# Performance work log

Hardware: AMD Instinct MI355X
Metric: run time of the kernel (lower is better)

Reference implementation:

```python
import jax, jax.numpy as jnp
import numpy as np

B, N, D = 2, 4096, 512
H, P = 8, 9            # num_heads, n_points
HD = D // H            # head_dim
OFFSET_SCALE = 4.0


def setup_inputs() -> dict:
    key = jax.random.key(0)
    ks = jax.random.split(key, 8)
    g = lambda k, shape, s: jax.random.normal(k, shape, jnp.float32) * s
    return {
        "x": jax.random.normal(ks[0], (B, N, D), jnp.float32),
        "Wq": g(ks[1], (D, D), 0.02),
        "bq": jnp.zeros((D,), jnp.float32),
        # offset predictor (original inits to zero; randomized small for a nontrivial test)
        "Woff": g(ks[2], (H * P * 2, D), 0.05),
        "boff": g(ks[3], (H * P * 2,), 0.05),
        # 1x1 conv producing k/v maps == a D -> 2D linear on tokens
        "Wkv": g(ks[4], (2 * D, D), 0.02),
        "bkv": jnp.zeros((2 * D,), jnp.float32),
        "Wo": g(ks[5], (D, D), 0.02),
        "bo": jnp.zeros((D,), jnp.float32),
        "h": 16,
        "w": 256,
    }


def _bilinear_zeros(feat, sx, sy, h, w):
    """grid_sample(mode=bilinear, padding=zeros, align_corners=True).
    feat: (B, H, N, hd) with N = h*w row-major; sx, sy: (B, H, S) pixel coords.
    Returns (B, H, S, hd). (align_corners=True normalize/denormalize round-trip
    in the original is the identity, so we sample at pixel coords directly.)
    """
    x0 = jnp.floor(sx)
    y0 = jnp.floor(sy)
    wx1 = sx - x0
    wy1 = sy - y0

    def corner(xi, yi, wgt):
        valid = ((xi >= 0) & (xi < w) & (yi >= 0) & (yi < h)).astype(feat.dtype)
        idx = (jnp.clip(yi, 0, h - 1) * w + jnp.clip(xi, 0, w - 1)).astype(jnp.int32)
        val = jnp.take_along_axis(feat, idx[..., None], axis=2)  # (B,H,S,hd)
        return val * (wgt * valid)[..., None]

    return (corner(x0, y0, (1 - wx1) * (1 - wy1))
            + corner(x0 + 1, y0, wx1 * (1 - wy1))
            + corner(x0, y0 + 1, (1 - wx1) * wy1)
            + corner(x0 + 1, y0 + 1, wx1 * wy1))


def reference(x, Wq, bq, Woff, boff, Wkv, bkv, Wo, bo, h, w):
    b, n, d = x.shape
    # queries, split heads -> (B,H,N,hd)
    q = (x @ Wq.T + bq).reshape(b, n, H, HD).transpose(0, 2, 1, 3)
    # per-query, per-head offsets in pixels: (B,N,H,P,2) (dx,dy)
    off = jnp.tanh(x @ Woff.T + boff).reshape(b, n, H, P, 2) * OFFSET_SCALE
    # 1x1 conv -> k/v token maps, split heads -> (B,H,N,hd)
    kv = x @ Wkv.T + bkv
    k = kv[..., :d].reshape(b, n, H, HD).transpose(0, 2, 1, 3)
    v = kv[..., d:].reshape(b, n, H, HD).transpose(0, 2, 1, 3)
    # base pixel grid (x,y) per token
    tok = jnp.arange(n)
    base = jnp.stack([(tok % w).astype(x.dtype), (tok // w).astype(x.dtype)], -1)  # (N,2)
    samp = base[None, :, None, None, :] + off          # (B,N,H,P,2)
    samp = samp.transpose(0, 2, 1, 3, 4).reshape(b, H, n * P, 2)
    sk = _bilinear_zeros(k, samp[..., 0], samp[..., 1], h, w).reshape(b, H, n, P, HD)
    sv = _bilinear_zeros(v, samp[..., 0], samp[..., 1], h, w).reshape(b, H, n, P, HD)
    logits = jnp.einsum('bhnd,bhnpd->bhnp', q, sk) * (HD ** -0.5)
    attn = jax.nn.softmax(logits, axis=-1)
    out = jnp.einsum('bhnp,bhnpd->bhnd', attn, sv)
    out = out.transpose(0, 2, 1, 3).reshape(b, n, d)   # merge heads
    return out @ Wo.T + bo
```

## Files before the change

### kernel.cpp

```cpp
#include <hip/hip_runtime.h>
#include <hip/hip_bf16.h>

static constexpr int B_  = 2;
static constexpr int N_  = 4096;
static constexpr int D_  = 512;
static constexpr int H_  = 8;
static constexpr int P_  = 9;
static constexpr int GH_ = 16;
static constexpr int GW_ = 256;
static constexpr int M_  = B_ * N_;

typedef __attribute__((ext_vector_type(8))) short bf16x8;
typedef __attribute__((ext_vector_type(4))) float f32x4;

__device__ __forceinline__ unsigned short f2b(float f) {
    __hip_bfloat16 h = __float2bfloat16(f);
    return *reinterpret_cast<unsigned short*>(&h);
}
__device__ __forceinline__ float b2f(unsigned short u) {
    return __uint_as_float(((unsigned int)u) << 16);
}
__device__ __forceinline__ float b2f_lo(unsigned int u) { return __uint_as_float(u << 16); }
__device__ __forceinline__ float b2f_hi(unsigned int u) { return __uint_as_float(u & 0xffff0000u); }

__global__ __launch_bounds__(256) void cast_multi(
    const float* __restrict__ x,   const float* __restrict__ wq,
    const float* __restrict__ wkv, const float* __restrict__ wo,
    const float* __restrict__ woff,
    unsigned short* __restrict__ x_hi, unsigned short* __restrict__ x_lo,
    unsigned short* __restrict__ wall, unsigned short* __restrict__ wob) {
    int g = blockIdx.x * 256 + threadIdx.x;

    if (g < 1048576) {
        float4 v = reinterpret_cast<const float4*>(x)[g];
        ushort4 hi, lo;
        hi.x = f2b(v.x); hi.y = f2b(v.y); hi.z = f2b(v.z); hi.w = f2b(v.w);
        lo.x = f2b(v.x - b2f(hi.x)); lo.y = f2b(v.y - b2f(hi.y));
        lo.z = f2b(v.z - b2f(hi.z)); lo.w = f2b(v.w - b2f(hi.w));
        reinterpret_cast<ushort4*>(x_hi)[g] = hi;
        reinterpret_cast<ushort4*>(x_lo)[g] = lo;
        return;
    }
    g -= 1048576;
    if (g < 65536) {
        float4 v = reinterpret_cast<const float4*>(wq)[g];
        ushort4 o; o.x = f2b(v.x); o.y = f2b(v.y); o.z = f2b(v.z); o.w = f2b(v.w);
        reinterpret_cast<ushort4*>(wall)[g] = o;
        return;
    }
    g -= 65536;
    if (g < 131072) {
        float4 v = reinterpret_cast<const float4*>(wkv)[g];
        ushort4 o; o.x = f2b(v.x); o.y = f2b(v.y); o.z = f2b(v.z); o.w = f2b(v.w);
        reinterpret_cast<ushort4*>(wall)[65536 + g] = o;
        return;
    }
    g -= 131072;
    if (g < 65536) {
        float4 v = reinterpret_cast<const float4*>(wo)[g];
        ushort4 o; o.x = f2b(v.x); o.y = f2b(v.y); o.z = f2b(v.z); o.w = f2b(v.w);
        reinterpret_cast<ushort4*>(wob)[g] = o;
        return;
    }
    g -= 65536;
    if (g < 18432) {
        float4 v = reinterpret_cast<const float4*>(woff)[g];
        ushort4 hi, lo;
        hi.x = f2b(v.x); hi.y = f2b(v.y); hi.z = f2b(v.z); hi.w = f2b(v.w);
        lo.x = f2b(v.x - b2f(hi.x)); lo.y = f2b(v.y - b2f(hi.y));
        lo.z = f2b(v.z - b2f(hi.z)); lo.w = f2b(v.w - b2f(hi.w));
        reinterpret_cast<ushort4*>(wall)[196608 + g] = hi;
        reinterpret_cast<ushort4*>(wall)[229376 + g] = lo;
        reinterpret_cast<ushort4*>(wall)[262144 + g] = hi;
        return;
    }
    g -= 18432;
    const int which = g / 14336;
    const int idx   = g - which * 14336;
    ushort4 z = {0, 0, 0, 0};
    reinterpret_cast<ushort4*>(wall)[215040 + which * 32768 + idx] = z;
}

__device__ __forceinline__ void gemm_seg(const unsigned short* __restrict__ A,
                                         const unsigned short* __restrict__ W,
                                         int m0, int n0, int Kloop, int lda, int ldw,
                                         short* As, short* Bs,
                                         f32x4 (&acc)[4][2], int wave, int lane) {
    const int gi = wave * 64 + lane;
    const int r0 = gi >> 2, c0 = (gi & 3) * 8;

    const unsigned short* pa0 = A + (size_t)(m0 + r0) * lda + c0;
    const unsigned short* pa1 = A + (size_t)(m0 + 64 + r0) * lda + c0;
    const unsigned short* pw  = W + (size_t)(n0 + r0) * ldw + c0;

    short* ldsA0 = As + wave * 512;
    short* ldsA1 = As + 2048 + wave * 512;
    short* ldsB  = Bs + wave * 512;

    const int wm = wave & 1, wn = wave >> 1;
    const int fr = lane & 15;
    const int fk = (lane >> 4) * 8;

    for (int k0 = 0; k0 < Kloop; k0 += 32) {
        __builtin_amdgcn_global_load_lds(
            (const __attribute__((address_space(1))) void*)(pa0 + k0),
            (__attribute__((address_space(3))) void*)ldsA0, 16, 0, 0);
        __builtin_amdgcn_global_load_lds(
            (const __attribute__((address_space(1))) void*)(pa1 + k0),
            (__attribute__((address_space(3))) void*)ldsA1, 16, 0, 0);
        __builtin_amdgcn_global_load_lds(
            (const __attribute__((address_space(1))) void*)(pw + k0),
            (__attribute__((address_space(3))) void*)ldsB, 16, 0, 0);
        __syncthreads();

        bf16x8 af[4], bf[2];
#pragma unroll
        for (int i = 0; i < 4; ++i)
            af[i] = *reinterpret_cast<const bf16x8*>(
                &As[(wm * 64 + i * 16 + fr) * 32 + fk]);
#pragma unroll
        for (int j = 0; j < 2; ++j)
            bf[j] = *reinterpret_cast<const bf16x8*>(
                &Bs[(wn * 32 + j * 16 + fr) * 32 + fk]);
#pragma unroll
        for (int i = 0; i < 4; ++i)
#pragma unroll
            for (int j = 0; j < 2; ++j)
                acc[i][j] = __builtin_amdgcn_mfma_f32_16x16x32_bf16(
                    af[i], bf[j], acc[i][j], 0, 0, 0);
        __syncthreads();
    }
}

__global__ __launch_bounds__(256, 3) void gemm_fused(
    const unsigned short* __restrict__ x_hi,
    const unsigned short* __restrict__ x_lo,
    const unsigned short* __restrict__ wall,
    const float* __restrict__ bq,
    const float* __restrict__ bkv,
    const float* __restrict__ boff,
    unsigned short* __restrict__ q_bf,
    unsigned short* __restrict__ k_bf,
    unsigned short* __restrict__ v_bf,
    float* __restrict__ off1,
    float* __restrict__ off2,
    float* __restrict__ off3) {
    __shared__ short As[4096];
    __shared__ short Bs[2048];
    const int t = threadIdx.x;
    const int wave = t >> 6, lane = t & 63;
    const int m0 = blockIdx.y * 128;
    const int n0 = blockIdx.x * 64;

    const unsigned short* A = (blockIdx.x >= 32) ? x_lo : x_hi;

    f32x4 acc[4][2] = {};
    gemm_seg(A, wall, m0, n0, 512, 512, 512, As, Bs, acc, wave, lane);

    const int wm = wave & 1, wn = wave >> 1;
    const int ecol = lane & 15;
    const int erow = (lane >> 4) * 4;
#pragma unroll
    for (int i = 0; i < 4; ++i) {
#pragma unroll
        for (int j = 0; j < 2; ++j) {
            const int n = n0 + wn * 32 + j * 16 + ecol;
#pragma unroll
            for (int r = 0; r < 4; ++r) {
                const int m = m0 + wm * 64 + i * 16 + erow + r;
                const float v = acc[i][j][r];
                if (n < 512) {
                    q_bf[(size_t)m * 512 + n] = f2b((v + bq[n]) * 0.125f);
                } else if (n < 1024) {
                    k_bf[(size_t)m * 512 + (n - 512)] = f2b(v + bkv[n - 512]);
                } else if (n < 1536) {
                    v_bf[(size_t)m * 512 + (n - 1024)] = f2b(v + bkv[n - 512]);
                } else if (n < 1792) {
                    const int c = n - 1536;
                    if (c < 144) off1[(size_t)m * 144 + c] = v + boff[c];
                } else if (n < 2048) {
                    const int c = n - 1792;
                    if (c < 144) off2[(size_t)m * 144 + c] = v;
                } else {
                    const int c = n - 2048;
                    if (c < 144) off3[(size_t)m * 144 + c] = v;
                }
            }
        }
    }
}

__global__ __launch_bounds__(256, 3) void gemm_out(
    const unsigned short* __restrict__ A,
    const unsigned short* __restrict__ W,
    const float* __restrict__ bias,
    float* __restrict__ out) {
    __shared__ short As[4096];
    __shared__ short Bs[2048];
    const int t = threadIdx.x;
    const int wave = t >> 6, lane = t & 63;
    const int m0 = blockIdx.y * 128;
    const int n0 = blockIdx.x * 64;

    f32x4 acc[4][2] = {};
    gemm_seg(A, W, m0, n0, 512, 512, 512, As, Bs, acc, wave, lane);

    const int wm = wave & 1, wn = wave >> 1;
    const int ecol = lane & 15;
    const int erow = (lane >> 4) * 4;
#pragma unroll
    for (int i = 0; i < 4; ++i) {
#pragma unroll
        for (int j = 0; j < 2; ++j) {
            const int n = n0 + wn * 32 + j * 16 + ecol;
            const float bb = bias[n];
#pragma unroll
            for (int r = 0; r < 4; ++r) {
                const int m = m0 + wm * 64 + i * 16 + erow + r;
                out[(size_t)m * 512 + n] = acc[i][j][r] + bb;
            }
        }
    }
}

__global__ __launch_bounds__(256) void samp_prep(const float* __restrict__ off1,
                                                 const float* __restrict__ off2,
                                                 const float* __restrict__ off3,
                                                 float4* __restrict__ sampw,
                                                 int4* __restrict__ sampo) {
    const int pid = blockIdx.x * 256 + threadIdx.x;
    int tmp = pid;
    const int p  = tmp % P_;  tmp /= P_;
    const int n  = tmp & (N_ - 1);
    const int bh = tmp >> 12;
    const int hh = bh & 7;
    const int b  = bh >> 3;

    const size_t tok = (size_t)b * N_ + n;
    const size_t oidx = tok * 144 + hh * 18 + 2 * p;
    const float2 a1 = *reinterpret_cast<const float2*>(off1 + oidx);
    const float2 a2 = *reinterpret_cast<const float2*>(off2 + oidx);
    const float2 a3 = *reinterpret_cast<const float2*>(off3 + oidx);
    const float dx = tanhf(a1.x + a2.x + a3.x) * 4.0f;
    const float dy = tanhf(a1.y + a2.y + a3.y) * 4.0f;
    const float sx = (float)(n & (GW_ - 1)) + dx;
    const float sy = (float)(n >> 8) + dy;
    const float x0f = floorf(sx), y0f = floorf(sy);
    const int x0 = (int)x0f, y0 = (int)y0f;
    const float wx1 = sx - x0f, wy1 = sy - y0f;
    const float wx0 = 1.0f - wx1, wy0 = 1.0f - wy1;

    float4 w;
    int4 ro;
    {
        const int xi = x0, yi = y0;
        const bool v = (xi >= 0) & (xi < GW_) & (yi >= 0) & (yi < GH_);
        w.x = v ? wx0 * wy0 : 0.0f;
        const int xc = xi < 0 ? 0 : (xi > 255 ? 255 : xi);
        const int yc = yi < 0 ? 0 : (yi > 15 ? 15 : yi);
        ro.x = (yc * GW_ + xc) * 512 + hh * 64;
    }
    {
        const int xi = x0 + 1, yi = y0;
        const bool v = (xi >= 0) & (xi < GW_) & (yi >= 0) & (yi < GH_);
        w.y = v ? wx1 * wy0 : 0.0f;
        const int xc = xi < 0 ? 0 : (xi > 255 ? 255 : xi);
        const int yc = yi < 0 ? 0 : (yi > 15 ? 15 : yi);
        ro.y = (yc * GW_ + xc) * 512 + hh * 64;
    }
    {
        const int xi = x0, yi = y0 + 1;
        const bool v = (xi >= 0) & (xi < GW_) & (yi >= 0) & (yi < GH_);
        w.z = v ? wx0 * wy1 : 0.0f;
        const int xc = xi < 0 ? 0 : (xi > 255 ? 255 : xi);
        const int yc = yi < 0 ? 0 : (yi > 15 ? 15 : yi);
        ro.z = (yc * GW_ + xc) * 512 + hh * 64;
    }
    {
        const int xi = x0 + 1, yi = y0 + 1;
        const bool v = (xi >= 0) & (xi < GW_) & (yi >= 0) & (yi < GH_);
        w.w = v ? wx1 * wy1 : 0.0f;
        const int xc = xi < 0 ? 0 : (xi > 255 ? 255 : xi);
        const int yc = yi < 0 ? 0 : (yi > 15 ? 15 : yi);
        ro.w = (yc * GW_ + xc) * 512 + hh * 64;
    }
    sampw[pid] = w;
    sampo[pid] = ro;
}

__global__ __launch_bounds__(256) void attn_sample(const unsigned short* __restrict__ q_bf,
                                                   const float4* __restrict__ sampw,
                                                   const int4* __restrict__ sampo,
                                                   const unsigned short* __restrict__ k_bf,
                                                   const unsigned short* __restrict__ v_bf,
                                                   unsigned short* __restrict__ a_bf) {
    const int lane = threadIdx.x & 63;
    const int quarter = lane >> 4;
    const int j    = lane & 15;
    const int wid  = blockIdx.x * 4 + (threadIdx.x >> 6);
    const int b    = wid >> 13;
    const int hh   = (wid >> 10) & 7;
    const int nq   = wid & 1023;
    const int n    = nq * 4 + quarter;

    const size_t tok = (size_t)b * N_ + n;
    const uint2 qp = *reinterpret_cast<const uint2*>(
        q_bf + tok * 512 + hh * 64 + 4 * j);
    const float q0 = b2f_lo(qp.x), q1 = b2f_hi(qp.x);
    const float q2 = b2f_lo(qp.y), q3 = b2f_hi(qp.y);

    const int pbase = ((b * H_ + hh) * N_ + n) * P_;
    const unsigned short* kbase = k_bf + (size_t)b * (N_ * 512) + 4 * j;
    const unsigned short* vbase = v_bf + (size_t)b * (N_ * 512) + 4 * j;

    float lg[9], s0[9], s1[9], s2[9], s3[9];
    float mx = -1e30f;

#pragma unroll
    for (int p = 0; p < P_; ++p) {
        const float4 w = sampw[pbase + p];
        const int4 ro = sampo[pbase + p];
        float k0 = 0.f, k1 = 0.f, k2 = 0.f, k3 = 0.f;
        float v0 = 0.f, v1 = 0.f, v2 = 0.f, v3 = 0.f;
#pragma unroll
        for (int c = 0; c < 4; ++c) {
            const int r = (c == 0) ? ro.x : (c == 1) ? ro.y : (c == 2) ? ro.z : ro.w;
            const float wgt = (c == 0) ? w.x : (c == 1) ? w.y : (c == 2) ? w.z : w.w;
            const uint2 ku = *reinterpret_cast<const uint2*>(kbase + r);
            const uint2 vu = *reinterpret_cast<const uint2*>(vbase + r);
            k0 = fmaf(wgt, b2f_lo(ku.x), k0); k1 = fmaf(wgt, b2f_hi(ku.x), k1);
            k2 = fmaf(wgt, b2f_lo(ku.y), k2); k3 = fmaf(wgt, b2f_hi(ku.y), k3);
            v0 = fmaf(wgt, b2f_lo(vu.x), v0); v1 = fmaf(wgt, b2f_hi(vu.x), v1);
            v2 = fmaf(wgt, b2f_lo(vu.y), v2); v3 = fmaf(wgt, b2f_hi(vu.y), v3);
        }
        float ts = fmaf(q0, k0, fmaf(q1, k1, fmaf(q2, k2, q3 * k3)));
#pragma unroll
        for (int s = 8; s > 0; s >>= 1) ts += __shfl_xor(ts, s, 64);
        lg[p] = ts;
        s0[p] = v0; s1[p] = v1; s2[p] = v2; s3[p] = v3;
        mx = fmaxf(mx, lg[p]);
    }

    float ssum = 0.f, o0 = 0.f, o1 = 0.f, o2 = 0.f, o3 = 0.f;
#pragma unroll
    for (int p = 0; p < P_; ++p) {
        const float e = __expf(lg[p] - mx);
        ssum += e;
        o0 = fmaf(e, s0[p], o0);
        o1 = fmaf(e, s1[p], o1);
        o2 = fmaf(e, s2[p], o2);
        o3 = fmaf(e, s3[p], o3);
    }
    const float rs = 1.0f / ssum;
    uint2 pack;
    pack.x = (unsigned int)f2b(o0 * rs) | ((unsigned int)f2b(o1 * rs) << 16);
    pack.y = (unsigned int)f2b(o2 * rs) | ((unsigned int)f2b(o3 * rs) << 16);
    *reinterpret_cast<uint2*>(a_bf + tok * 512 + hh * 64 + 4 * j) = pack;
}

extern "C" void kernel_launch(void* const* d_in, const int* in_sizes, int n_in,
                              void* d_out, int out_size, void* d_ws, size_t ws_size,
                              hipStream_t stream) {
    const float* x    = (const float*)d_in[0];
    const float* bq   = (const float*)d_in[2];
    const float* Woff = (const float*)d_in[3];
    const float* boff = (const float*)d_in[4];
    const float* bkv  = (const float*)d_in[6];
    const float* bo   = (const float*)d_in[8];
    float* out = (float*)d_out;

    char* ws = (char*)d_ws;
    unsigned short* q_bf    = (unsigned short*)ws; ws += (size_t)M_ * 512 * 2;
    unsigned short* k_bf    = (unsigned short*)ws; ws += (size_t)M_ * 512 * 2;
    unsigned short* v_bf    = (unsigned short*)ws; ws += (size_t)M_ * 512 * 2;
    float*          off1    = (float*)ws;          ws += (size_t)M_ * 144 * 4;
    float*          off2    = (float*)ws;          ws += (size_t)M_ * 144 * 4;
    float*          off3    = (float*)ws;          ws += (size_t)M_ * 144 * 4;
    unsigned short* xlo_abf = (unsigned short*)ws; ws += (size_t)M_ * 512 * 2;
    unsigned short* x_hi    = (unsigned short*)ws; ws += (size_t)M_ * 512 * 2;
    unsigned short* wall    = (unsigned short*)ws; ws += (size_t)2304 * 512 * 2;
    unsigned short* wob     = (unsigned short*)ws; ws += (size_t)512 * 512 * 2;
    float4*         sampw   = (float4*)ws;         ws += (size_t)M_ * H_ * P_ * 16;
    int4*           sampo   = (int4*)ws;           ws += (size_t)M_ * H_ * P_ * 16;

    const dim3 blk(256);

    cast_multi<<<dim3(5360), blk, 0, stream>>>(
        x, (const float*)d_in[1], (const float*)d_in[5], (const float*)d_in[7], Woff,
        x_hi, xlo_abf, wall, wob);

    gemm_fused<<<dim3(36, M_ / 128), blk, 0, stream>>>(
        x_hi, xlo_abf, wall, bq, bkv, boff, q_bf, k_bf, v_bf, off1, off2, off3);

    samp_prep<<<dim3(M_ * H_ * P_ / 256), blk, 0, stream>>>(
        off1, off2, off3, sampw, sampo);

    attn_sample<<<dim3((B_ * H_ * N_) / 16), blk, 0, stream>>>(
        q_bf, sampw, sampo, k_bf, v_bf, xlo_abf);

    gemm_out<<<dim3(8, M_ / 128), blk, 0, stream>>>(xlo_abf, wob, bo, out);
}
```

Baseline: 200.3 us.

## Fuse sampling-prep into attention kernel and deepen GEMM K-step to 64

The separate samp_prep kernel is removed. Each wave of attn_sample now computes its 36 bilinear weight/offset sets from the raw offset partial sums directly into LDS, which drops a launch and the write and re-read of about 19 MB of sampw/sampo. Separately, the GEMM inner loop now loads two 32-wide K slices per barrier pair (K step 64), halving the number of syncthreads at the cost of doubling LDS per block. The added __syncthreads and serialized prep in attn_sample, and the larger LDS footprint, may reduce occupancy.

```diff
diff --git a/kernel.cpp b/kernel.cpp
--- a/kernel.cpp
+++ b/kernel.cpp
@@ -93,41 +93,46 @@
     const unsigned short* pa1 = A + (size_t)(m0 + 64 + r0) * lda + c0;
     const unsigned short* pw  = W + (size_t)(n0 + r0) * ldw + c0;
 
-    short* ldsA0 = As + wave * 512;
-    short* ldsA1 = As + 2048 + wave * 512;
-    short* ldsB  = Bs + wave * 512;
-
     const int wm = wave & 1, wn = wave >> 1;
     const int fr = lane & 15;
     const int fk = (lane >> 4) * 8;
 
-    for (int k0 = 0; k0 < Kloop; k0 += 32) {
-        __builtin_amdgcn_global_load_lds(
-            (const __attribute__((address_space(1))) void*)(pa0 + k0),
-            (__attribute__((address_space(3))) void*)ldsA0, 16, 0, 0);
-        __builtin_amdgcn_global_load_lds(
-            (const __attribute__((address_space(1))) void*)(pa1 + k0),
-            (__attribute__((address_space(3))) void*)ldsA1, 16, 0, 0);
-        __builtin_amdgcn_global_load_lds(
-            (const __attribute__((address_space(1))) void*)(pw + k0),
-            (__attribute__((address_space(3))) void*)ldsB, 16, 0, 0);
+    for (int k0 = 0; k0 < Kloop; k0 += 64) {
+#pragma unroll
+        for (int t = 0; t < 2; ++t) {
+            __builtin_amdgcn_global_load_lds(
+                (const __attribute__((address_space(1))) void*)(pa0 + k0 + t * 32),
+                (__attribute__((address_space(3))) void*)(As + t * 4096 + wave * 512),
+                16, 0, 0);
+            __builtin_amdgcn_global_load_lds(
+                (const __attribute__((address_space(1))) void*)(pa1 + k0 + t * 32),
+                (__attribute__((address_space(3))) void*)(As + t * 4096 + 2048 + wave * 512),
+                16, 0, 0);
+            __builtin_amdgcn_global_load_lds(
+                (const __attribute__((address_space(1))) void*)(pw + k0 + t * 32),
+                (__attribute__((address_space(3))) void*)(Bs + t * 2048 + wave * 512),
+                16, 0, 0);
+        }
         __syncthreads();
 
-        bf16x8 af[4], bf[2];
-#pragma unroll
-        for (int i = 0; i < 4; ++i)
-            af[i] = *reinterpret_cast<const bf16x8*>(
-                &As[(wm * 64 + i * 16 + fr) * 32 + fk]);
-#pragma unroll
-        for (int j = 0; j < 2; ++j)
-            bf[j] = *reinterpret_cast<const bf16x8*>(
-                &Bs[(wn * 32 + j * 16 + fr) * 32 + fk]);
-#pragma unroll
-        for (int i = 0; i < 4; ++i)
+#pragma unroll
+        for (int t = 0; t < 2; ++t) {
+            bf16x8 af[4], bf[2];
+#pragma unroll
+            for (int i = 0; i < 4; ++i)
+                af[i] = *reinterpret_cast<const bf16x8*>(
+                    &As[t * 4096 + (wm * 64 + i * 16 + fr) * 32 + fk]);
 #pragma unroll
             for (int j = 0; j < 2; ++j)
-                acc[i][j] = __builtin_amdgcn_mfma_f32_16x16x32_bf16(
-                    af[i], bf[j], acc[i][j], 0, 0, 0);
+                bf[j] = *reinterpret_cast<const bf16x8*>(
+                    &Bs[t * 2048 + (wn * 32 + j * 16 + fr) * 32 + fk]);
+#pragma unroll
+            for (int i = 0; i < 4; ++i)
+#pragma unroll
+                for (int j = 0; j < 2; ++j)
+                    acc[i][j] = __builtin_amdgcn_mfma_f32_16x16x32_bf16(
+                        af[i], bf[j], acc[i][j], 0, 0, 0);
+        }
         __syncthreads();
     }
 }
@@ -145,8 +150,8 @@
     float* __restrict__ off1,
     float* __restrict__ off2,
     float* __restrict__ off3) {
-    __shared__ short As[4096];
-    __shared__ short Bs[2048];
+    __shared__ short As[8192];
+    __shared__ short Bs[4096];
     const int t = threadIdx.x;
     const int wave = t >> 6, lane = t & 63;
     const int m0 = blockIdx.y * 128;
@@ -195,8 +200,8 @@
     const unsigned short* __restrict__ W,
     const float* __restrict__ bias,
     float* __restrict__ out) {
-    __shared__ short As[4096];
-    __shared__ short Bs[2048];
+    __shared__ short As[8192];
+    __shared__ short Bs[4096];
     const int t = threadIdx.x;
     const int wave = t >> 6, lane = t & 63;
     const int m0 = blockIdx.y * 128;
@@ -223,85 +228,82 @@
     }
 }
 
-__global__ __launch_bounds__(256) void samp_prep(const float* __restrict__ off1,
-                                                 const float* __restrict__ off2,
-                                                 const float* __restrict__ off3,
-                                                 float4* __restrict__ sampw,
-                                                 int4* __restrict__ sampo) {
-    const int pid = blockIdx.x * 256 + threadIdx.x;
-    int tmp = pid;
-    const int p  = tmp % P_;  tmp /= P_;
-    const int n  = tmp & (N_ - 1);
-    const int bh = tmp >> 12;
-    const int hh = bh & 7;
-    const int b  = bh >> 3;
-
-    const size_t tok = (size_t)b * N_ + n;
-    const size_t oidx = tok * 144 + hh * 18 + 2 * p;
-    const float2 a1 = *reinterpret_cast<const float2*>(off1 + oidx);
-    const float2 a2 = *reinterpret_cast<const float2*>(off2 + oidx);
-    const float2 a3 = *reinterpret_cast<const float2*>(off3 + oidx);
-    const float dx = tanhf(a1.x + a2.x + a3.x) * 4.0f;
-    const float dy = tanhf(a1.y + a2.y + a3.y) * 4.0f;
-    const float sx = (float)(n & (GW_ - 1)) + dx;
-    const float sy = (float)(n >> 8) + dy;
-    const float x0f = floorf(sx), y0f = floorf(sy);
-    const int x0 = (int)x0f, y0 = (int)y0f;
-    const float wx1 = sx - x0f, wy1 = sy - y0f;
-    const float wx0 = 1.0f - wx1, wy0 = 1.0f - wy1;
-
-    float4 w;
-    int4 ro;
-    {
-        const int xi = x0, yi = y0;
-        const bool v = (xi >= 0) & (xi < GW_) & (yi >= 0) & (yi < GH_);
-        w.x = v ? wx0 * wy0 : 0.0f;
-        const int xc = xi < 0 ? 0 : (xi > 255 ? 255 : xi);
-        const int yc = yi < 0 ? 0 : (yi > 15 ? 15 : yi);
-        ro.x = (yc * GW_ + xc) * 512 + hh * 64;
-    }
-    {
-        const int xi = x0 + 1, yi = y0;
-        const bool v = (xi >= 0) & (xi < GW_) & (yi >= 0) & (yi < GH_);
-        w.y = v ? wx1 * wy0 : 0.0f;
-        const int xc = xi < 0 ? 0 : (xi > 255 ? 255 : xi);
-        const int yc = yi < 0 ? 0 : (yi > 15 ? 15 : yi);
-        ro.y = (yc * GW_ + xc) * 512 + hh * 64;
-    }
-    {
-        const int xi = x0, yi = y0 + 1;
-        const bool v = (xi >= 0) & (xi < GW_) & (yi >= 0) & (yi < GH_);
-        w.z = v ? wx0 * wy1 : 0.0f;
-        const int xc = xi < 0 ? 0 : (xi > 255 ? 255 : xi);
-        const int yc = yi < 0 ? 0 : (yi > 15 ? 15 : yi);
-        ro.z = (yc * GW_ + xc) * 512 + hh * 64;
-    }
-    {
-        const int xi = x0 + 1, yi = y0 + 1;
-        const bool v = (xi >= 0) & (xi < GW_) & (yi >= 0) & (yi < GH_);
-        w.w = v ? wx1 * wy1 : 0.0f;
-        const int xc = xi < 0 ? 0 : (xi > 255 ? 255 : xi);
-        const int yc = yi < 0 ? 0 : (yi > 15 ? 15 : yi);
-        ro.w = (yc * GW_ + xc) * 512 + hh * 64;
-    }
-    sampw[pid] = w;
-    sampo[pid] = ro;
-}
-
 __global__ __launch_bounds__(256) void attn_sample(const unsigned short* __restrict__ q_bf,
-                                                   const float4* __restrict__ sampw,
-                                                   const int4* __restrict__ sampo,
+                                                   const float* __restrict__ off1,
+                                                   const float* __restrict__ off2,
+                                                   const float* __restrict__ off3,
                                                    const unsigned short* __restrict__ k_bf,
                                                    const unsigned short* __restrict__ v_bf,
                                                    unsigned short* __restrict__ a_bf) {
+    __shared__ float4 pw_s[4][36];
+    __shared__ int4   po_s[4][36];
+
     const int lane = threadIdx.x & 63;
+    const int wave = threadIdx.x >> 6;
     const int quarter = lane >> 4;
     const int j    = lane & 15;
-    const int wid  = blockIdx.x * 4 + (threadIdx.x >> 6);
+    const int wid  = blockIdx.x * 4 + wave;
     const int b    = wid >> 13;
     const int hh   = (wid >> 10) & 7;
     const int nq   = wid & 1023;
     const int n    = nq * 4 + quarter;
+
+    if (lane < 36) {
+        const int qt = lane / 9;
+        const int p  = lane - qt * 9;
+        const int tn = nq * 4 + qt;
+        const size_t tokq = (size_t)b * N_ + tn;
+        const size_t oidx = tokq * 144 + hh * 18 + 2 * p;
+        const float2 a1 = *reinterpret_cast<const float2*>(off1 + oidx);
+        const float2 a2 = *reinterpret_cast<const float2*>(off2 + oidx);
+        const float2 a3 = *reinterpret_cast<const float2*>(off3 + oidx);
+        const float dx = tanhf(a1.x + a2.x + a3.x) * 4.0f;
+        const float dy = tanhf(a1.y + a2.y + a3.y) * 4.0f;
+        const float sx = (float)(tn & (GW_ - 1)) + dx;
+        const float sy = (float)(tn >> 8) + dy;
+        const float x0f = floorf(sx), y0f = floorf(sy);
+        const int x0 = (int)x0f, y0 = (int)y0f;
+        const float wx1 = sx - x0f, wy1 = sy - y0f;
+        const float wx0 = 1.0f - wx1, wy0 = 1.0f - wy1;
+
+        float4 w;
+        int4 ro;
+        {
+            const int xi = x0, yi = y0;
+            const bool v = (xi >= 0) & (xi < GW_) & (yi >= 0) & (yi < GH_);
+            w.x = v ? wx0 * wy0 : 0.0f;
+            const int xc = xi < 0 ? 0 : (xi > 255 ? 255 : xi);
+            const int yc = yi < 0 ? 0 : (yi > 15 ? 15 : yi);
+            ro.x = (yc * GW_ + xc) * 512 + hh * 64;
+        }
+        {
+            const int xi = x0 + 1, yi = y0;
+            const bool v = (xi >= 0) & (xi < GW_) & (yi >= 0) & (yi < GH_);
+            w.y = v ? wx1 * wy0 : 0.0f;
+            const int xc = xi < 0 ? 0 : (xi > 255 ? 255 : xi);
+            const int yc = yi < 0 ? 0 : (yi > 15 ? 15 : yi);
+            ro.y = (yc * GW_ + xc) * 512 + hh * 64;
+        }
+        {
+            const int xi = x0, yi = y0 + 1;
+            const bool v = (xi >= 0) & (xi < GW_) & (yi >= 0) & (yi < GH_);
+            w.z = v ? wx0 * wy1 : 0.0f;
+            const int xc = xi < 0 ? 0 : (xi > 255 ? 255 : xi);
+            const int yc = yi < 0 ? 0 : (yi > 15 ? 15 : yi);
+            ro.z = (yc * GW_ + xc) * 512 + hh * 64;
+        }
+        {
+            const int xi = x0 + 1, yi = y0 + 1;
+            const bool v = (xi >= 0) & (xi < GW_) & (yi >= 0) & (yi < GH_);
+            w.w = v ? wx1 * wy1 : 0.0f;
+            const int xc = xi < 0 ? 0 : (xi > 255 ? 255 : xi);
+            const int yc = yi < 0 ? 0 : (yi > 15 ? 15 : yi);
+            ro.w = (yc * GW_ + xc) * 512 + hh * 64;
+        }
+        pw_s[wave][lane] = w;
+        po_s[wave][lane] = ro;
+    }
+    __syncthreads();
 
     const size_t tok = (size_t)b * N_ + n;
     const uint2 qp = *reinterpret_cast<const uint2*>(
@@ -309,17 +311,17 @@
     const float q0 = b2f_lo(qp.x), q1 = b2f_hi(qp.x);
     const float q2 = b2f_lo(qp.y), q3 = b2f_hi(qp.y);
 
-    const int pbase = ((b * H_ + hh) * N_ + n) * P_;
     const unsigned short* kbase = k_bf + (size_t)b * (N_ * 512) + 4 * j;
     const unsigned short* vbase = v_bf + (size_t)b * (N_ * 512) + 4 * j;
+    const int ebase = quarter * 9;
 
     float lg[9], s0[9], s1[9], s2[9], s3[9];
     float mx = -1e30f;
 
 #pragma unroll
     for (int p = 0; p < P_; ++p) {
-        const float4 w = sampw[pbase + p];
-        const int4 ro = sampo[pbase + p];
+        const float4 w = pw_s[wave][ebase + p];
+        const int4 ro = po_s[wave][ebase + p];
         float k0 = 0.f, k1 = 0.f, k2 = 0.f, k3 = 0.f;
         float v0 = 0.f, v1 = 0.f, v2 = 0.f, v3 = 0.f;
 #pragma unroll
@@ -380,8 +382,6 @@
     unsigned short* x_hi    = (unsigned short*)ws; ws += (size_t)M_ * 512 * 2;
     unsigned short* wall    = (unsigned short*)ws; ws += (size_t)2304 * 512 * 2;
     unsigned short* wob     = (unsigned short*)ws; ws += (size_t)512 * 512 * 2;
-    float4*         sampw   = (float4*)ws;         ws += (size_t)M_ * H_ * P_ * 16;
-    int4*           sampo   = (int4*)ws;           ws += (size_t)M_ * H_ * P_ * 16;
 
     const dim3 blk(256);
 
@@ -392,11 +392,8 @@
     gemm_fused<<<dim3(36, M_ / 128), blk, 0, stream>>>(
         x_hi, xlo_abf, wall, bq, bkv, boff, q_bf, k_bf, v_bf, off1, off2, off3);
 
-    samp_prep<<<dim3(M_ * H_ * P_ / 256), blk, 0, stream>>>(
-        off1, off2, off3, sampw, sampo);
-
     attn_sample<<<dim3((B_ * H_ * N_) / 16), blk, 0, stream>>>(
-        q_bf, sampw, sampo, k_bf, v_bf, xlo_abf);
+        q_bf, off1, off2, off3, k_bf, v_bf, xlo_abf);
 
     gemm_out<<<dim3(8, M_ / 128), blk, 0, stream>>>(xlo_abf, wob, bo, out);
 }
```

Measured after the change: 180.5 us. 1.11x faster.
